# Optimization experiments

Measured on AMD Instinct MI355X. Metric: run time of the kernel, lower is better.

The kernel has to match this reference:

```python
import jax, jax.numpy as jnp
import numpy as np

B, S, D, H = 4, 1024, 1024, 16
DH = D // H
NEG = -10000.0  # mask fill value for non-float32 (bool) masks in the torch code


def setup_inputs() -> dict:
    key = jax.random.key(0)
    ks = jax.random.split(key, 16)
    scale = 0.02
    inp = {
        "query": jax.random.normal(ks[0], (B, S, D), jnp.float32),
        "key": jax.random.normal(ks[1], (B, S, D), jnp.float32),
        "value": jax.random.normal(ks[2], (B, S, D), jnp.float32),
        "pos_embedding": jax.random.normal(ks[3], (B, S, D), jnp.float32),
        # learned params (torch Linear convention: y = x @ W.T + b, W is (out,in))
        "Wq": jax.random.normal(ks[4], (D, D), jnp.float32) * scale,
        "bq": jnp.zeros((D,), jnp.float32),
        "Wk": jax.random.normal(ks[5], (D, D), jnp.float32) * scale,
        "bk": jnp.zeros((D,), jnp.float32),
        "Wv": jax.random.normal(ks[6], (D, D), jnp.float32) * scale,
        "bv": jnp.zeros((D,), jnp.float32),
        "Wpos": jax.random.normal(ks[7], (D, D), jnp.float32) * scale,
        "u_bias": jax.random.normal(ks[8], (H, DH), jnp.float32) * scale,
        "v_bias": jax.random.normal(ks[9], (H, DH), jnp.float32) * scale,
        "Wout": jax.random.normal(ks[10], (D, D), jnp.float32) * scale,
        "bout": jnp.zeros((D,), jnp.float32),
    }
    # right-padding mask: lengths in [S//2, S]; mask[b,i,j] = pad(i) | pad(j)
    lengths = jax.random.randint(ks[11], (B,), S // 2, S + 1)
    pad = jnp.arange(S)[None, :] >= lengths[:, None]  # (B,S)
    inp["mask"] = pad[:, :, None] | pad[:, None, :]  # (B,S,S) bool
    return inp


def _relative_shift(pos_score, mask):
    """Batch-safe Transformer-XL relative shift (vectorized version of the
    per-batch python loop). pos_score: (B,H,S,S), mask: (B,S,S) bool."""
    b, h, s, _ = pos_score.shape
    # per-row true length: S - number of padded rows (column 0 is never padded)
    L = s - jnp.sum(mask[:, :, 0].astype(jnp.int32), axis=-1)  # (B,)
    i = jnp.arange(s)[:, None]
    j = jnp.arange(s)[None, :]

    def shift_one(ps, Lb):  # ps: (H,S,S), Lb: scalar int
        # padded[h,r,0]=0; padded[h,r,k]=ps[h,r,k-1]; flat index of out[i,j] in
        # the (Lb+1, Lb) reshape of padded[:, :Lb, :Lb+1], rows 1: -> offset Lb
        m = Lb + i * Lb + j            # (S,S)
        row = m // (Lb + 1)
        col = m % (Lb + 1)
        g = ps[:, jnp.clip(row, 0, s - 1), jnp.clip(col - 1, 0, s - 1)]  # (H,S,S)
        valid = (i < Lb) & (j < Lb) & (col != 0)
        return jnp.where(valid[None], g, jnp.zeros((), ps.dtype))

    shifted = jax.vmap(shift_one)(pos_score, L)
    # masked_fill_(padding_mask, 0.0)
    return jnp.where(mask[:, None, :, :], jnp.zeros((), pos_score.dtype), shifted)


def reference(query, key, value, pos_embedding, mask,
              Wq, bq, Wk, bk, Wv, bv, Wpos, u_bias, v_bias, Wout, bout):
    b = query.shape[0]
    sqrt_dim = np.sqrt(D).astype(np.float32)

    q = (query @ Wq.T + bq).reshape(b, -1, H, DH)                 # (B,S,H,dh)
    k = (key @ Wk.T + bk).reshape(b, -1, H, DH)                   # (B,S,H,dh)
    v = (value @ Wv.T + bv).reshape(b, -1, H, DH)                 # (B,S,H,dh)
    p = (pos_embedding @ Wpos.T).reshape(b, -1, H, DH)            # (B,S,H,dh)

    content_score = jnp.einsum('bqhd,bkhd->bhqk', q + u_bias, k)  # (B,H,S,S)
    pos_score = jnp.einsum('bqhd,bkhd->bhqk', q + v_bias, p)      # (B,H,S,S)
    pos_score = _relative_shift(pos_score, mask)

    score = (content_score + pos_score) / sqrt_dim
    m4 = mask[:, None, :, :]
    score = jnp.where(m4, NEG, score)
    attn = jax.nn.softmax(score, axis=-1)
    attn = jnp.where(m4, jnp.zeros((), attn.dtype), attn)
    # dropout is identity in eval mode
    context = jnp.einsum('bhqk,bkhd->bqhd', attn, v).reshape(b, -1, D)
    return context @ Wout.T + bout
```

## Files before the change

kernel.cpp:

```cpp
#include <hip/hip_runtime.h>

#define B_ 4
#define S_ 1024
#define D_ 1024
#define H_ 16
#define DH_ 64
#define OOS 0.03125f

#define QPL (1088 * 64)
#define KPL (1024 * 64)
#define VPL (1024 * 64)
#define PPL (200 * 1024)
#define PADLO 1056

#define APL_SW (256 * 32 * 512)
#define WPL_SW (64 * 32 * 512)

typedef __attribute__((ext_vector_type(8))) short short8;
typedef __attribute__((ext_vector_type(4))) float f32x4;
typedef const __attribute__((address_space(1))) unsigned int* gas_t;
typedef __attribute__((address_space(3))) unsigned int* las_t;

__device__ __forceinline__ ushort f2bf(float x) {
  unsigned u = __float_as_uint(x);
  unsigned r = u + 0x7fffu + ((u >> 16) & 1u);
  return (ushort)(r >> 16);
}
__device__ __forceinline__ float bf2f(ushort u) {
  return __uint_as_float(((unsigned)u) << 16);
}

union pack8 { ushort u[8]; uint4 v; };

struct ConvDesc { const float* src; ushort* hi; ushort* lo; };
struct ConvArgs { ConvDesc d[5]; };

__global__ __launch_bounds__(256) void conv_split(ConvArgs args)
{
  const ConvDesc dd = args.d[blockIdx.y];
  const int tt = blockIdx.x;
  const int tid = threadIdx.x;
  const float* src = dd.src + (size_t)tt * 16 * 1024;
  ushort* hi = dd.hi + (size_t)tt * 32 * 512;
  ushort* lo = dd.lo + (size_t)tt * 32 * 512;
#pragma unroll 4
  for (int q = 0; q < 16; ++q) {
    const int s = q * 256 + tid;
    const int r = s >> 8, c4 = s & 255;
    const float4 x = *(const float4*)(src + r * 1024 + c4 * 4);
    const int k = c4 * 4;
    const size_t addr = (size_t)(k >> 5) * 512 + ((k & 31) >> 3) * 128 + r * 8 + (k & 7);
    ushort4 hu, lu;
    hu.x = f2bf(x.x); lu.x = f2bf(x.x - bf2f(hu.x));
    hu.y = f2bf(x.y); lu.y = f2bf(x.y - bf2f(hu.y));
    hu.z = f2bf(x.z); lu.z = f2bf(x.z - bf2f(hu.z));
    hu.w = f2bf(x.w); lu.w = f2bf(x.w - bf2f(hu.w));
    *(ushort4*)(hi + addr) = hu;
    *(ushort4*)(lo + addr) = lu;
  }
}

struct GemmDesc {
  const ushort* Ahi; const ushort* Alo;
  const ushort* Bhi; const ushort* Blo;
  const float* bias; ushort* O1; ushort* O2;
  const float* ub; const float* vb; int mode; int pad;
};
struct GemmArgs { GemmDesc g[4]; };

__global__ __launch_bounds__(256, 2) void gemm_fused(GemmArgs args)
{
  __shared__ __align__(16) ushort SM[16384];
  const int lid = blockIdx.x + 8 * blockIdx.y + 256 * blockIdx.z;
  const int swz = (lid & 7) * 128 + (lid >> 3);
  const int bx = swz & 7;
  const int by = (swz >> 3) & 31;
  const int bz = swz >> 8;

  const GemmDesc g = args.g[bz];
  const int tid = threadIdx.x;
  const int wave = tid >> 6, lane = tid & 63;
  const int m16 = lane & 15, quad = lane >> 4;
  const int mw2 = wave & 1, nw2 = wave >> 1;
  const int mt0 = by * 8;
  const int nt0 = bx * 8;

  f32x4 acc[4][4];
#pragma unroll
  for (int mf = 0; mf < 4; ++mf)
#pragma unroll
    for (int nf = 0; nf < 4; ++nf) acc[mf][nf] = (f32x4){0.f, 0.f, 0.f, 0.f};

  for (int kb = 0; kb < 32; ++kb) {
    __syncthreads();
    for (int t = wave; t < 32; t += 4) {
      const ushort* gp;
      int l;
      if (t < 8)       { gp = g.Ahi + ((size_t)(mt0 + t) * 32 + kb) * 512;       l = t * 512; }
      else if (t < 16) { gp = g.Alo + ((size_t)(mt0 + t - 8) * 32 + kb) * 512;   l = 4096 + (t - 8) * 512; }
      else if (t < 24) { gp = g.Bhi + ((size_t)(nt0 + t - 16) * 32 + kb) * 512;  l = 8192 + (t - 16) * 512; }
      else             { gp = g.Blo + ((size_t)(nt0 + t - 24) * 32 + kb) * 512;  l = 12288 + (t - 24) * 512; }
      __builtin_amdgcn_global_load_lds((gas_t)(gp + lane * 8), (las_t)(SM + l), 16, 0, 0);
    }
    __syncthreads();
    short8 ah[4], al[4], bh[4], bl[4];
#pragma unroll
    for (int mf = 0; mf < 4; ++mf) {
      ah[mf] = *(const short8*)(SM + (mw2 * 4 + mf) * 512 + lane * 8);
      al[mf] = *(const short8*)(SM + 4096 + (mw2 * 4 + mf) * 512 + lane * 8);
    }
#pragma unroll
    for (int nf = 0; nf < 4; ++nf) {
      bh[nf] = *(const short8*)(SM + 8192 + (nw2 * 4 + nf) * 512 + lane * 8);
      bl[nf] = *(const short8*)(SM + 12288 + (nw2 * 4 + nf) * 512 + lane * 8);
    }
#pragma unroll
    for (int mf = 0; mf < 4; ++mf)
#pragma unroll
      for (int nf = 0; nf < 4; ++nf) {
        acc[mf][nf] = __builtin_amdgcn_mfma_f32_16x16x32_bf16(ah[mf], bh[nf], acc[mf][nf], 0, 0, 0);
        acc[mf][nf] = __builtin_amdgcn_mfma_f32_16x16x32_bf16(ah[mf], bl[nf], acc[mf][nf], 0, 0, 0);
        acc[mf][nf] = __builtin_amdgcn_mfma_f32_16x16x32_bf16(al[mf], bh[nf], acc[mf][nf], 0, 0, 0);
      }
  }

  const int Mb = by * 128, Nb = bx * 128;
  float* const E0 = (float*)SM;
  float* const E1 = (float*)(SM + 8192);
#pragma unroll
  for (int p = 0; p < 2; ++p) {
    __syncthreads();
    if (mw2 == p) {
      float* const E = nw2 ? E1 : E0;
#pragma unroll
      for (int mf = 0; mf < 4; ++mf)
#pragma unroll
        for (int nf = 0; nf < 4; ++nf)
#pragma unroll
          for (int reg = 0; reg < 4; ++reg)
            E[(mf * 16 + quad * 4 + reg) * 64 + nf * 16 + m16] = acc[mf][nf][reg];
    }
    __syncthreads();

#pragma unroll
    for (int cpart = 0; cpart < 2; ++cpart) {
      float* const E = cpart ? E1 : E0;
      const int tokBase = Mb + p * 64;
      const int nBase = Nb + cpart * 64;

      if (g.mode == 3) {
#pragma unroll
        for (int q = 0; q < 2; ++q) {
          const int s = tid + 256 * q;
          const int cc = s & 63, rg = s >> 6;
          const int tok0 = tokBase + rg * 8;
          const int n = nBase + cc;
          const int bb = tok0 >> 10, jr = tok0 & 1023;
          const int jt = jr >> 6, ksj = (jr >> 5) & 1, qk = (jr >> 3) & 3;
          const int h = n >> 6, dd = n & 63;
          const int subd = dd >> 4, nn = dd & 15;
          const size_t base = (size_t)(bb * 16 + h) * VPL + (size_t)jt * 4096 +
                              (size_t)(subd * 2 + ksj) * 512 + (qk * 16 + nn) * 8;
          const float bvv = g.bias[n];
          pack8 pk;
#pragma unroll
          for (int i = 0; i < 8; ++i) pk.u[i] = f2bf(E[(rg * 8 + i) * 64 + cc] + bvv);
          *(uint4*)(g.O1 + base) = pk.v;
        }
      } else {
#pragma unroll
        for (int q = 0; q < 2; ++q) {
          const int s = tid + 256 * q;
          const int r = s >> 3, gc = s & 7;
          const int token = tokBase + r;
          const int n = nBase + gc * 8;
          float v[8];
          *(float4*)&v[0] = *(const float4*)&E[r * 64 + gc * 8];
          *(float4*)&v[4] = *(const float4*)&E[r * 64 + gc * 8 + 4];
          if (g.mode == 1) {
            const int bb = token >> 10, sr = token & 1023;
            const int h = n >> 6, d = n & 63;
            const size_t base = (size_t)(bb * 16 + h) * QPL + (size_t)sr * 64 + d;
            pack8 pu, pv;
#pragma unroll
            for (int j = 0; j < 8; ++j) {
              const float qv_ = v[j] + g.bias[n + j];
              pu.u[j] = f2bf(qv_ + g.ub[n + j]);
              pv.u[j] = f2bf(qv_ + g.vb[n + j]);
            }
            *(uint4*)(g.O1 + base) = pu.v;
            *(uint4*)(g.O2 + base) = pv.v;
          } else {
            const int bb = token >> 10, jr = token & 1023;
            const int h = n >> 6, dd = n & 63;
            const int ks = dd >> 5, qk = (dd >> 3) & 3;
            size_t base;
            if (g.mode == 2)
              base = (size_t)(bb * 16 + h) * KPL + (size_t)(jr >> 6) * 4096 +
                     (size_t)((((jr >> 4) & 3) * 2 + ks)) * 512 + (qk * 16 + (jr & 15)) * 8;
            else {
              const int ro = jr + PADLO;
              base = (size_t)(bb * 16 + h) * PPL + (size_t)(ro >> 4) * 1024 +
                     (size_t)ks * 512 + (qk * 16 + (ro & 15)) * 8;
            }
            pack8 pk;
#pragma unroll
            for (int j = 0; j < 8; ++j)
              pk.u[j] = f2bf(v[j] + (g.mode == 2 ? g.bias[n + j] : 0.f));
            *(uint4*)(g.O1 + base) = pk.v;
          }
        }
      }
    }
  }
}

__global__ __launch_bounds__(256, 2) void gemm_out(
    const ushort* __restrict__ Ahi, const ushort* __restrict__ Alo,
    const ushort* __restrict__ Bhi, const ushort* __restrict__ Blo,
    const float* __restrict__ bias, float* __restrict__ C)
{
  __shared__ __align__(16) ushort SM[12288];
  const int tid = threadIdx.x;
  const int wave = tid >> 6, lane = tid & 63;
  const int m16 = lane & 15, quad = lane >> 4;
  const int mw2 = wave & 1, nw2 = wave >> 1;
  const int mt0 = blockIdx.y * 4;
  const int nt0 = blockIdx.x * 8;

  f32x4 acc[2][4];
#pragma unroll
  for (int mf = 0; mf < 2; ++mf)
#pragma unroll
    for (int nf = 0; nf < 4; ++nf) acc[mf][nf] = (f32x4){0.f, 0.f, 0.f, 0.f};

  for (int kb = 0; kb < 32; ++kb) {
    __syncthreads();
    for (int t = wave; t < 24; t += 4) {
      const ushort* g;
      int l;
      if (t < 4)       { g = Ahi + ((size_t)(mt0 + t) * 32 + kb) * 512;      l = t * 512; }
      else if (t < 8)  { g = Alo + ((size_t)(mt0 + t - 4) * 32 + kb) * 512;  l = 2048 + (t - 4) * 512; }
      else if (t < 16) { g = Bhi + ((size_t)(nt0 + t - 8) * 32 + kb) * 512;  l = 4096 + (t - 8) * 512; }
      else             { g = Blo + ((size_t)(nt0 + t - 16) * 32 + kb) * 512; l = 8192 + (t - 16) * 512; }
      __builtin_amdgcn_global_load_lds((gas_t)(g + lane * 8), (las_t)(SM + l), 16, 0, 0);
    }
    __syncthreads();
    short8 ah[2], al[2], bh[4], bl[4];
#pragma unroll
    for (int mf = 0; mf < 2; ++mf) {
      ah[mf] = *(const short8*)(SM + (mw2 * 2 + mf) * 512 + lane * 8);
      al[mf] = *(const short8*)(SM + 2048 + (mw2 * 2 + mf) * 512 + lane * 8);
    }
#pragma unroll
    for (int nf = 0; nf < 4; ++nf) {
      bh[nf] = *(const short8*)(SM + 4096 + (nw2 * 4 + nf) * 512 + lane * 8);
      bl[nf] = *(const short8*)(SM + 8192 + (nw2 * 4 + nf) * 512 + lane * 8);
    }
#pragma unroll
    for (int mf = 0; mf < 2; ++mf)
#pragma unroll
      for (int nf = 0; nf < 4; ++nf) {
        acc[mf][nf] = __builtin_amdgcn_mfma_f32_16x16x32_bf16(ah[mf], bh[nf], acc[mf][nf], 0, 0, 0);
        acc[mf][nf] = __builtin_amdgcn_mfma_f32_16x16x32_bf16(ah[mf], bl[nf], acc[mf][nf], 0, 0, 0);
        acc[mf][nf] = __builtin_amdgcn_mfma_f32_16x16x32_bf16(al[mf], bh[nf], acc[mf][nf], 0, 0, 0);
      }
  }

  const int Mb = blockIdx.y * 64, Nb = blockIdx.x * 128;
  float* const E = (float*)SM;
#pragma unroll
  for (int c = 0; c < 2; ++c) {
    __syncthreads();
    if (nw2 == c) {
#pragma unroll
      for (int mf = 0; mf < 2; ++mf)
#pragma unroll
        for (int nf = 0; nf < 4; ++nf)
#pragma unroll
          for (int reg = 0; reg < 4; ++reg)
            E[(mw2 * 32 + mf * 16 + quad * 4 + reg) * 64 + nf * 16 + m16] = acc[mf][nf][reg];
    }
    __syncthreads();
#pragma unroll
    for (int q = 0; q < 2; ++q) {
      const int s = tid + 256 * q;
      const int r = s >> 3, g = s & 7;
      const int token = Mb + r;
      const int n = Nb + c * 64 + g * 8;
      float v[8];
      *(float4*)&v[0] = *(const float4*)&E[r * 64 + g * 8];
      *(float4*)&v[4] = *(const float4*)&E[r * 64 + g * 8 + 4];
      float4 o0, o1;
      o0.x = v[0] + bias[n + 0]; o0.y = v[1] + bias[n + 1];
      o0.z = v[2] + bias[n + 2]; o0.w = v[3] + bias[n + 3];
      o1.x = v[4] + bias[n + 4]; o1.y = v[5] + bias[n + 5];
      o1.z = v[6] + bias[n + 6]; o1.w = v[7] + bias[n + 7];
      *(float4*)(C + (size_t)token * 1024 + n) = o0;
      *(float4*)(C + (size_t)token * 1024 + n + 4) = o1;
    }
  }
}

__global__ void len_kernel(const int* __restrict__ mask, int* __restrict__ len,
                           ushort* __restrict__ Psw)
{
  const int b = blockIdx.x;
  int cnt = 0;
  for (int i = threadIdx.x; i < S_; i += 256)
    cnt += (mask[(size_t)b * S_ * S_ + (size_t)i * S_] != 0) ? 1 : 0;
  __shared__ int sh[256];
  sh[threadIdx.x] = cnt;
  __syncthreads();
  for (int off = 128; off > 0; off >>= 1) {
    if (threadIdx.x < off) sh[threadIdx.x] += sh[threadIdx.x + off];
    __syncthreads();
  }
  if (threadIdx.x == 0) len[b] = S_ - sh[0];
  for (int idx = threadIdx.x; idx < 16 * 64; idx += 256) {
    const int h = idx >> 6, d = idx & 63;
    Psw[(size_t)(b * 16 + h) * PPL + 65 * 1024 + (d >> 5) * 512 +
        (((d >> 3) & 3) * 16 + 15) * 8 + (d & 7)] = 0;
  }
}

__global__ __launch_bounds__(512, 4) void attn_mfma2(
    const ushort* __restrict__ Qu, const ushort* __restrict__ Qv,
    const ushort* __restrict__ Ksw, const ushort* __restrict__ Vsw,
    const ushort* __restrict__ Psw, const int* __restrict__ len,
    float* __restrict__ CTX)
{
  __shared__ __align__(16) ushort SMEM[26624];
  __shared__ float mrow[64], lrow[64], arow[64];

  ushort* const Ks_  = SMEM;
  ushort* const Vts_ = SMEM + 4096;
  ushort* const P1s_ = SMEM + 8192;
  ushort* const P2s_ = SMEM + 17408;
  float*  const sc   = (float*)(SMEM + 8192);
  ushort* const Pb   = SMEM + 17408;

  const int tid  = threadIdx.x;
  const int wave = tid >> 6, lane = tid & 63;
  const int hw   = wave >> 2, w4 = wave & 3;
  const int m16  = lane & 15, quad = lane >> 4;
  const int mw   = w4 & 1,  nw   = w4 >> 1;
  const int koff0 = quad * 8;

  const int base = blockIdx.x * 64;
  const int i0 = base + hw * 32;
  const int h  = blockIdx.y;
  const int b  = blockIdx.z;
  const int ph = b * 16 + h;
  const int L  = len[b];
  const size_t gb = ((size_t)b * S_) * D_ + h * DH_;

  if (base >= L) {
    for (int idx = tid; idx < 64 * 64; idx += 512) {
      const int r = idx >> 6, d = idx & 63;
      CTX[gb + (size_t)(base + r) * D_ + d] = 0.f;
    }
    return;
  }
  const bool active = (i0 < L);

  const ushort* quP = Qu + (size_t)ph * QPL;
  const ushort* qvP = Qv + (size_t)ph * QPL;
  short8 qufr[2][2], qvfr[2][2][2];
#pragma unroll
  for (int Mt = 0; Mt < 2; ++Mt)
#pragma unroll
    for (int ks = 0; ks < 2; ++ks) {
      qufr[Mt][ks] = *(const short8*)(quP + (size_t)(i0 + 16 * Mt + m16) * 64 + ks * 32 + koff0);
#pragma unroll
      for (int off = 0; off < 2; ++off)
        qvfr[off][Mt][ks] =
            *(const short8*)(qvP + (size_t)(i0 + off + 16 * Mt + m16) * 64 + ks * 32 + koff0);
    }

  if (tid < 64) { mrow[tid] = -3.0e38f; lrow[tid] = 0.f; arow[tid] = 0.f; }

  f32x4 ctx0 = {0.f, 0.f, 0.f, 0.f}, ctx1 = {0.f, 0.f, 0.f, 0.f};

  const ushort* ksP = Ksw + (size_t)ph * KPL;
  const ushort* vsP = Vsw + (size_t)ph * VPL;
  const ushort* psP = Psw + (size_t)ph * PPL;

  for (int j0 = 0; j0 < L; j0 += 64) {
    __syncthreads();

    const int jt = j0 >> 6;
    const int A1 = L - 32 - i0 + j0, A2 = j0 - i0 - 33;
    const int ro1 = A1 + PADLO, ro2 = A2 + PADLO;
    const int rb1 = ro1 >> 4, rb2 = ro2 >> 4;
    const int d1 = ro1 & 15, d2 = ro2 & 15;
    const int rb1lo = (L - 64 - base + j0 + PADLO) >> 4;
    const int rb2lo = (j0 - base - 65 + PADLO) >> 4;
    const ushort* P1h = P1s_ + ((rb1 - rb1lo) << 10);
    const ushort* P2h = P2s_ + ((rb2 - rb2lo) << 10);

    {
      const ushort* kgo = ksP + (size_t)jt * 4096;
      const ushort* vgo = vsP + (size_t)jt * 4096;
      const ushort* p1o = psP + (size_t)rb1lo * 1024;
      const ushort* p2o = psP + (size_t)rb2lo * 1024;
      for (int t = wave; t < 52; t += 8) {
        const ushort* g;
        int l;
        if (t < 8)       { g = kgo + t * 512;        l = t * 512; }
        else if (t < 16) { g = vgo + (t - 8) * 512;  l = 4096 + (t - 8) * 512; }
        else if (t < 34) { g = p1o + (t - 16) * 512; l = 8192 + (t - 16) * 512; }
        else             { g = p2o + (t - 34) * 512; l = 17408 + (t - 34) * 512; }
        __builtin_amdgcn_global_load_lds((gas_t)(g + lane * 8), (las_t)(SMEM + l), 16, 0, 0);
      }
    }
    __syncthreads();

    const int jrem = L - j0;
    const int jmax = (jrem < 64) ? jrem : 64;
    const int cthr = 31 + i0 - j0;

    f32x4 av[9];
#pragma unroll
    for (int t = 0; t < 9; ++t) {
      const int id = w4 + 4 * t;
      f32x4 a = {0.f, 0.f, 0.f, 0.f};
      if (active) {
        if (id < 8) {
          const int Mt = id & 1, Nt = id >> 1;
          if (16 * Nt < jmax) {
            const ushort* bp = Ks_ + (Nt * 2) * 512 + lane * 8;
            a = __builtin_amdgcn_mfma_f32_16x16x32_bf16(qufr[Mt][0], *(const short8*)bp, a, 0, 0, 0);
            a = __builtin_amdgcn_mfma_f32_16x16x32_bf16(qufr[Mt][1], *(const short8*)(bp + 512), a, 0, 0, 0);
          }
        } else if (id < 22) {
          const int e = id - 8, Mt = e & 1, Ntp = e >> 1;
          const int sm = 16 * (Ntp + Mt);
          if (sm >= d1 + 1 && sm <= jmax + d1 + 30 && 16 * Ntp - d1 <= cthr) {
            const ushort* bp = P1h + (Ntp * 2) * 512 + lane * 8;
            a = __builtin_amdgcn_mfma_f32_16x16x32_bf16(qvfr[0][Mt][0], *(const short8*)bp, a, 0, 0, 0);
            a = __builtin_amdgcn_mfma_f32_16x16x32_bf16(qvfr[0][Mt][1], *(const short8*)(bp + 512), a, 0, 0, 0);
          }
        } else {
          const int e = id - 22, Mt = e & 1, Ntp = e >> 1;
          const int sm = 16 * (Ntp + Mt);
          if (sm >= d2 + 1 && sm <= jmax + d2 + 30 && 16 * Ntp + 15 - d2 > cthr) {
            const ushort* bp = P2h + (Ntp * 2) * 512 + lane * 8;
            a = __builtin_amdgcn_mfma_f32_16x16x32_bf16(qvfr[1][Mt][0], *(const short8*)bp, a, 0, 0, 0);
            a = __builtin_amdgcn_mfma_f32_16x16x32_bf16(qvfr[1][Mt][1], *(const short8*)(bp + 512), a, 0, 0, 0);
          }
        }
      }
      av[t] = a;
    }
    __syncthreads();

#pragma unroll
    for (int t = 0; t < 2; ++t) {
      const int id = w4 + 4 * t;
      if (id < 8) {
        const int Mt = id & 1, Nt = id >> 1;
        if (16 * Nt < jmax) {
#pragma unroll
          for (int reg = 0; reg < 4; ++reg)
            sc[(hw * 32 + 16 * Mt + quad * 4 + reg) * 68 + 16 * Nt + m16] =
                active ? av[t][reg] : 0.f;
        }
      }
    }
    __syncthreads();

    if (active) {
#pragma unroll
      for (int t = 0; t < 9; ++t) {
        const int id = w4 + 4 * t;
        if (id >= 8) {
          const bool isG2 = id >= 22;
          const int e = id - (isG2 ? 22 : 8), Mt = e & 1, Ntp = e >> 1;
          const int dl = isG2 ? d2 : d1;
          const int sm = 16 * (Ntp + Mt);
          const bool use = sm >= dl + 1 && sm <= jmax + dl + 30 &&
                           (isG2 ? (16 * Ntp + 15 - dl > cthr) : (16 * Ntp - dl <= cthr));
          if (use) {
            const int c = 16 * Ntp + m16 - dl;
            const bool sel = isG2 ? (c > cthr) : (c <= cthr);
            if (sel) {
#pragma unroll
              for (int reg = 0; reg < 4; ++reg) {
                const int il = 16 * Mt + quad * 4 + reg;
                const int jl = c - 31 + il;
                if (jl >= 0 && jl < 64) sc[(hw * 32 + il) * 68 + jl] += av[t][reg];
              }
            }
          }
        }
      }
    }
    __syncthreads();

    {
      const int row = tid >> 3, t8 = tid & 7, jb = t8 * 8;
      const float* sr = sc + row * 68 + jb;
      float mx = -3.0e38f;
#pragma unroll
      for (int q = 0; q < 8; ++q)
        if (jb + q < jmax) mx = fmaxf(mx, sr[q]);
#pragma unroll
      for (int off = 1; off < 8; off <<= 1)
        mx = fmaxf(mx, __shfl_xor(mx, off, 64));
      if (t8 == 0) {
        const float mo = mrow[row];
        const float mn = fmaxf(mo, mx);
        arow[row] = __expf((mo - mn) * OOS);
        mrow[row] = mn;
      }
    }
    __syncthreads();
    {
      const int row = tid >> 3, t8 = tid & 7, jb = t8 * 8;
      const float m = mrow[row];
      const float* sr = sc + row * 68 + jb;
      float e[8], s = 0.f;
#pragma unroll
      for (int q = 0; q < 8; ++q) {
        float v = 0.f;
        if (jb + q < jmax) v = __expf((sr[q] - m) * OOS);
        e[q] = v;
        s += v;
      }
      ushort4 u0, u1;
      u0.x = f2bf(e[0]); u0.y = f2bf(e[1]); u0.z = f2bf(e[2]); u0.w = f2bf(e[3]);
      u1.x = f2bf(e[4]); u1.y = f2bf(e[5]); u1.z = f2bf(e[6]); u1.w = f2bf(e[7]);
      *(ushort4*)&Pb[row * 72 + jb] = u0;
      *(ushort4*)&Pb[row * 72 + jb + 4] = u1;
#pragma unroll
      for (int off = 1; off < 8; off <<= 1) s += __shfl_xor(s, off, 64);
      if (t8 == 0) lrow[row] = lrow[row] * arow[row] + s;
    }
    __syncthreads();

    if (active) {
      float al[4];
#pragma unroll
      for (int reg = 0; reg < 4; ++reg) al[reg] = arow[hw * 32 + 16 * mw + quad * 4 + reg];
#pragma unroll
      for (int reg = 0; reg < 4; ++reg) { ctx0[reg] *= al[reg]; ctx1[reg] *= al[reg]; }
      const ushort* ap = Pb + (hw * 32 + 16 * mw + m16) * 72;
#pragma unroll
      for (int ksj = 0; ksj < 2; ++ksj) {
        const short8 a = *(const short8*)(ap + ksj * 32 + koff0);
        ctx0 = __builtin_amdgcn_mfma_f32_16x16x32_bf16(
            a, *(const short8*)(Vts_ + ((nw * 2) * 2 + ksj) * 512 + lane * 8), ctx0, 0, 0, 0);
        ctx1 = __builtin_amdgcn_mfma_f32_16x16x32_bf16(
            a, *(const short8*)(Vts_ + ((nw * 2 + 1) * 2 + ksj) * 512 + lane * 8), ctx1, 0, 0, 0);
      }
    }
  }

#pragma unroll
  for (int reg = 0; reg < 4; ++reg) {
    const int il = 16 * mw + quad * 4 + reg;
    const int gi = i0 + il;
    const float inv = (active && gi < L) ? (1.f / lrow[hw * 32 + il]) : 0.f;
    CTX[gb + (size_t)gi * D_ + nw * 32 + m16]      = ctx0[reg] * inv;
    CTX[gb + (size_t)gi * D_ + nw * 32 + 16 + m16] = ctx1[reg] * inv;
  }
}

extern "C" void kernel_launch(void* const* d_in, const int* in_sizes, int n_in,
                              void* d_out, int out_size, void* d_ws, size_t ws_size,
                              hipStream_t stream)
{
  (void)in_sizes; (void)n_in; (void)out_size;
  const float* query = (const float*)d_in[0];
  const float* key   = (const float*)d_in[1];
  const float* value = (const float*)d_in[2];
  const float* pos   = (const float*)d_in[3];
  const float* Wq    = (const float*)d_in[4];
  const float* bq    = (const float*)d_in[5];
  const float* Wk    = (const float*)d_in[6];
  const float* bk    = (const float*)d_in[7];
  const float* Wv    = (const float*)d_in[8];
  const float* bv    = (const float*)d_in[9];
  const float* Wpos  = (const float*)d_in[10];
  const float* ub    = (const float*)d_in[11];
  const float* vb    = (const float*)d_in[12];
  const float* Wout  = (const float*)d_in[13];
  const float* bout  = (const float*)d_in[14];
  const int*   mask  = (const int*)d_in[15];

  char* cur = (char*)d_ws;
  auto take = [&](size_t bytes) {
    char* p = cur;
    cur += (bytes + 255) & ~(size_t)255;
    return p;
  };
  float*  CTX = (float*)take((size_t)4096 * 1024 * 4);
  ushort* Qu  = (ushort*)take((size_t)64 * QPL * 2);
  ushort* Qv  = (ushort*)take((size_t)64 * QPL * 2);
  ushort* Ksw = (ushort*)take((size_t)64 * KPL * 2);
  ushort* Vsw = (ushort*)take((size_t)64 * VPL * 2);
  ushort* Psw = (ushort*)take((size_t)64 * PPL * 2);
  ushort* Ah[4], *Al[4];
  for (int i = 0; i < 4; ++i) {
    Ah[i] = (ushort*)take((size_t)APL_SW * 2);
    Al[i] = (ushort*)take((size_t)APL_SW * 2);
  }
  ushort* Wh[5], *Wl[5];
  for (int i = 0; i < 5; ++i) {
    Wh[i] = (ushort*)take((size_t)WPL_SW * 2);
    Wl[i] = (ushort*)take((size_t)WPL_SW * 2);
  }
  int* len = (int*)take(256);
  ushort* Ch = Ah[0];
  ushort* Cl = Al[0];
  if (ws_size < (size_t)(cur - (char*)d_ws)) return;

  len_kernel<<<dim3(B_), dim3(256), 0, stream>>>(mask, len, Psw);

  {
    ConvArgs a;
    a.d[0] = {query, Ah[0], Al[0]};
    a.d[1] = {key,   Ah[1], Al[1]};
    a.d[2] = {value, Ah[2], Al[2]};
    a.d[3] = {pos,   Ah[3], Al[3]};
    a.d[4] = {query, Ah[0], Al[0]};
    conv_split<<<dim3(256, 4), dim3(256), 0, stream>>>(a);
    ConvArgs w;
    w.d[0] = {Wq,   Wh[0], Wl[0]};
    w.d[1] = {Wk,   Wh[1], Wl[1]};
    w.d[2] = {Wv,   Wh[2], Wl[2]};
    w.d[3] = {Wpos, Wh[3], Wl[3]};
    w.d[4] = {Wout, Wh[4], Wl[4]};
    conv_split<<<dim3(64, 5), dim3(256), 0, stream>>>(w);
  }

  {
    GemmArgs ga;
    ga.g[0] = {Ah[0], Al[0], Wh[0], Wl[0], bq, Qu, Qv, ub, vb, 1, 0};
    ga.g[1] = {Ah[1], Al[1], Wh[1], Wl[1], bk, Ksw, nullptr, nullptr, nullptr, 2, 0};
    ga.g[2] = {Ah[2], Al[2], Wh[2], Wl[2], bv, Vsw, nullptr, nullptr, nullptr, 3, 0};
    ga.g[3] = {Ah[3], Al[3], Wh[3], Wl[3], nullptr, Psw, nullptr, nullptr, nullptr, 4, 0};
    gemm_fused<<<dim3(8, 32, 4), dim3(256), 0, stream>>>(ga);
  }

  attn_mfma2<<<dim3(S_ / 64, H_, B_), dim3(512), 0, stream>>>(
      Qu, Qv, Ksw, Vsw, Psw, len, CTX);

  {
    ConvArgs c;
    c.d[0] = {CTX, Ch, Cl};
    c.d[1] = c.d[0]; c.d[2] = c.d[0]; c.d[3] = c.d[0]; c.d[4] = c.d[0];
    conv_split<<<dim3(256, 1), dim3(256), 0, stream>>>(c);
  }

  gemm_out<<<dim3(8, 64), dim3(256), 0, stream>>>(Ch, Cl, Wh[4], Wl[4], bout,
                                                  (float*)d_out);
}
```

Baseline: 662.6 us.

## Double-buffer LDS tiles in projection and output GEMMs to overlap loads

```diff
diff --git a/kernel.cpp b/kernel.cpp
--- a/kernel.cpp
+++ b/kernel.cpp
@@ -70,7 +70,7 @@
 
 __global__ __launch_bounds__(256, 2) void gemm_fused(GemmArgs args)
 {
-  __shared__ __align__(16) ushort SM[16384];
+  __shared__ __align__(16) ushort SM[32768];
   const int lid = blockIdx.x + 8 * blockIdx.y + 256 * blockIdx.z;
   const int swz = (lid & 7) * 128 + (lid >> 3);
   const int bx = swz & 7;
@@ -85,14 +85,7 @@
   const int mt0 = by * 8;
   const int nt0 = bx * 8;
 
-  f32x4 acc[4][4];
-#pragma unroll
-  for (int mf = 0; mf < 4; ++mf)
-#pragma unroll
-    for (int nf = 0; nf < 4; ++nf) acc[mf][nf] = (f32x4){0.f, 0.f, 0.f, 0.f};
-
-  for (int kb = 0; kb < 32; ++kb) {
-    __syncthreads();
+  auto stage = [&](int kb, ushort* buf) {
     for (int t = wave; t < 32; t += 4) {
       const ushort* gp;
       int l;
@@ -100,19 +93,33 @@
       else if (t < 16) { gp = g.Alo + ((size_t)(mt0 + t - 8) * 32 + kb) * 512;   l = 4096 + (t - 8) * 512; }
       else if (t < 24) { gp = g.Bhi + ((size_t)(nt0 + t - 16) * 32 + kb) * 512;  l = 8192 + (t - 16) * 512; }
       else             { gp = g.Blo + ((size_t)(nt0 + t - 24) * 32 + kb) * 512;  l = 12288 + (t - 24) * 512; }
-      __builtin_amdgcn_global_load_lds((gas_t)(gp + lane * 8), (las_t)(SM + l), 16, 0, 0);
-    }
-    __syncthreads();
+      __builtin_amdgcn_global_load_lds((gas_t)(gp + lane * 8), (las_t)(buf + l), 16, 0, 0);
+    }
+  };
+
+  f32x4 acc[4][4];
+#pragma unroll
+  for (int mf = 0; mf < 4; ++mf)
+#pragma unroll
+    for (int nf = 0; nf < 4; ++nf) acc[mf][nf] = (f32x4){0.f, 0.f, 0.f, 0.f};
+
+  stage(0, SM);
+  __syncthreads();
+
+  for (int kb = 0; kb < 32; ++kb) {
+    ushort* const curb = SM + ((kb & 1) << 14);
+    if (kb + 1 < 32) stage(kb + 1, SM + (((kb + 1) & 1) << 14));
+
     short8 ah[4], al[4], bh[4], bl[4];
 #pragma unroll
     for (int mf = 0; mf < 4; ++mf) {
-      ah[mf] = *(const short8*)(SM + (mw2 * 4 + mf) * 512 + lane * 8);
-      al[mf] = *(const short8*)(SM + 4096 + (mw2 * 4 + mf) * 512 + lane * 8);
+      ah[mf] = *(const short8*)(curb + (mw2 * 4 + mf) * 512 + lane * 8);
+      al[mf] = *(const short8*)(curb + 4096 + (mw2 * 4 + mf) * 512 + lane * 8);
     }
 #pragma unroll
     for (int nf = 0; nf < 4; ++nf) {
-      bh[nf] = *(const short8*)(SM + 8192 + (nw2 * 4 + nf) * 512 + lane * 8);
-      bl[nf] = *(const short8*)(SM + 12288 + (nw2 * 4 + nf) * 512 + lane * 8);
+      bh[nf] = *(const short8*)(curb + 8192 + (nw2 * 4 + nf) * 512 + lane * 8);
+      bl[nf] = *(const short8*)(curb + 12288 + (nw2 * 4 + nf) * 512 + lane * 8);
     }
 #pragma unroll
     for (int mf = 0; mf < 4; ++mf)
@@ -122,6 +129,7 @@
         acc[mf][nf] = __builtin_amdgcn_mfma_f32_16x16x32_bf16(ah[mf], bl[nf], acc[mf][nf], 0, 0, 0);
         acc[mf][nf] = __builtin_amdgcn_mfma_f32_16x16x32_bf16(al[mf], bh[nf], acc[mf][nf], 0, 0, 0);
       }
+    __syncthreads();
   }
 
   const int Mb = by * 128, Nb = bx * 128;
@@ -220,7 +228,7 @@
     const ushort* __restrict__ Bhi, const ushort* __restrict__ Blo,
     const float* __restrict__ bias, float* __restrict__ C)
 {
-  __shared__ __align__(16) ushort SM[12288];
+  __shared__ __align__(16) ushort SM[24576];
   const int tid = threadIdx.x;
   const int wave = tid >> 6, lane = tid & 63;
   const int m16 = lane & 15, quad = lane >> 4;
@@ -228,14 +236,7 @@
   const int mt0 = blockIdx.y * 4;
   const int nt0 = blockIdx.x * 8;
 
-  f32x4 acc[2][4];
-#pragma unroll
-  for (int mf = 0; mf < 2; ++mf)
-#pragma unroll
-    for (int nf = 0; nf < 4; ++nf) acc[mf][nf] = (f32x4){0.f, 0.f, 0.f, 0.f};
-
-  for (int kb = 0; kb < 32; ++kb) {
-    __syncthreads();
+  auto stage = [&](int kb, ushort* buf) {
     for (int t = wave; t < 24; t += 4) {
       const ushort* g;
       int l;
@@ -243,19 +244,33 @@
       else if (t < 8)  { g = Alo + ((size_t)(mt0 + t - 4) * 32 + kb) * 512;  l = 2048 + (t - 4) * 512; }
       else if (t < 16) { g = Bhi + ((size_t)(nt0 + t - 8) * 32 + kb) * 512;  l = 4096 + (t - 8) * 512; }
       else             { g = Blo + ((size_t)(nt0 + t - 16) * 32 + kb) * 512; l = 8192 + (t - 16) * 512; }
-      __builtin_amdgcn_global_load_lds((gas_t)(g + lane * 8), (las_t)(SM + l), 16, 0, 0);
-    }
-    __syncthreads();
+      __builtin_amdgcn_global_load_lds((gas_t)(g + lane * 8), (las_t)(buf + l), 16, 0, 0);
+    }
+  };
+
+  f32x4 acc[2][4];
+#pragma unroll
+  for (int mf = 0; mf < 2; ++mf)
+#pragma unroll
+    for (int nf = 0; nf < 4; ++nf) acc[mf][nf] = (f32x4){0.f, 0.f, 0.f, 0.f};
+
+  stage(0, SM);
+  __syncthreads();
+
+  for (int kb = 0; kb < 32; ++kb) {
+    ushort* const curb = SM + (kb & 1) * 12288;
+    if (kb + 1 < 32) stage(kb + 1, SM + ((kb + 1) & 1) * 12288);
+
     short8 ah[2], al[2], bh[4], bl[4];
 #pragma unroll
     for (int mf = 0; mf < 2; ++mf) {
-      ah[mf] = *(const short8*)(SM + (mw2 * 2 + mf) * 512 + lane * 8);
-      al[mf] = *(const short8*)(SM + 2048 + (mw2 * 2 + mf) * 512 + lane * 8);
+      ah[mf] = *(const short8*)(curb + (mw2 * 2 + mf) * 512 + lane * 8);
+      al[mf] = *(const short8*)(curb + 2048 + (mw2 * 2 + mf) * 512 + lane * 8);
     }
 #pragma unroll
     for (int nf = 0; nf < 4; ++nf) {
-      bh[nf] = *(const short8*)(SM + 4096 + (nw2 * 4 + nf) * 512 + lane * 8);
-      bl[nf] = *(const short8*)(SM + 8192 + (nw2 * 4 + nf) * 512 + lane * 8);
+      bh[nf] = *(const short8*)(curb + 4096 + (nw2 * 4 + nf) * 512 + lane * 8);
+      bl[nf] = *(const short8*)(curb + 8192 + (nw2 * 4 + nf) * 512 + lane * 8);
     }
 #pragma unroll
     for (int mf = 0; mf < 2; ++mf)
@@ -265,6 +280,7 @@
         acc[mf][nf] = __builtin_amdgcn_mfma_f32_16x16x32_bf16(ah[mf], bl[nf], acc[mf][nf], 0, 0, 0);
         acc[mf][nf] = __builtin_amdgcn_mfma_f32_16x16x32_bf16(al[mf], bh[nf], acc[mf][nf], 0, 0, 0);
       }
+    __syncthreads();
   }
 
   const int Mb = blockIdx.y * 64, Nb = blockIdx.x * 128;
```

Result: no change. 669.7 us (+1.1%).
